# Kernel optimization log

Hardware: AMD Instinct MI355X
Metric: run time of the kernel (lower is better)

Reference implementation:

```python
import jax, jax.numpy as jnp
import numpy as np

D_MODEL, H, DK = 768, 12, 64
RQ, RK, RV = 6, 2, 2
B, S = 8, 4096


def setup_inputs() -> dict:
    key = jax.random.key(0)
    ks = jax.random.split(key, 16)
    def lin(k, din, dout):
        k1, k2 = jax.random.split(k)
        s = 1.0 / np.sqrt(din)
        W = jax.random.uniform(k1, (din, dout), jnp.float32, -s, s)
        b = jax.random.uniform(k2, (dout,), jnp.float32, -s, s)
        return W, b
    W_a_q, b_a_q = lin(ks[0], D_MODEL, H * RQ)
    W_b_q, b_b_q = lin(ks[1], D_MODEL, DK * RQ)
    W_a_k, b_a_k = lin(ks[2], D_MODEL, H * RK)
    W_b_k, b_b_k = lin(ks[3], D_MODEL, DK * RK)
    W_a_v, b_a_v = lin(ks[4], D_MODEL, H * RV)
    W_b_v, b_b_v = lin(ks[5], D_MODEL, DK * RV)
    W_out, b_out = lin(ks[6], H * DK, D_MODEL)
    x = jax.random.normal(ks[7], (B, S, D_MODEL), jnp.float32)
    rope_pos = jax.random.normal(ks[8], (S, DK), jnp.float32)
    return {
        "x": x, "rope_pos": rope_pos,
        "W_a_q": W_a_q, "b_a_q": b_a_q, "W_b_q": W_b_q, "b_b_q": b_b_q,
        "W_a_k": W_a_k, "b_a_k": b_a_k, "W_b_k": W_b_k, "b_b_k": b_b_k,
        "W_a_v": W_a_v, "b_a_v": b_a_v, "W_b_v": W_b_v, "b_b_v": b_b_v,
        "W_out": W_out, "b_out": b_out,
    }


def reference(x, rope_pos, W_a_q, b_a_q, W_b_q, b_b_q, W_a_k, b_a_k,
              W_b_k, b_b_k, W_a_v, b_a_v, W_b_v, b_b_v, W_out, b_out):
    b, s, _ = x.shape
    # factor projections; layout (B, S, rank, feature)
    A_Q = (x @ W_a_q + b_a_q).reshape(b, s, RQ, H)
    B_Q = (x @ W_b_q + b_b_q).reshape(b, s, RQ, DK)
    A_K = (x @ W_a_k + b_a_k).reshape(b, s, RK, H)
    B_K = (x @ W_b_k + b_b_k).reshape(b, s, RK, DK)
    A_V = (x @ W_a_v + b_a_v).reshape(b, s, RV, H)
    B_V = (x @ W_b_v + b_b_v).reshape(b, s, RV, DK)
    rope = rope_pos[None, :, None, :]  # (1,S,1,DK)
    B_Q = B_Q * rope
    B_K = B_K * rope
    # rank-sum outer products -> (B,S,H,DK)
    Q = jnp.einsum('bsrh,bsrd->bshd', A_Q, B_Q)
    K = jnp.einsum('bsrh,bsrd->bshd', A_K, B_K)
    V = jnp.einsum('bsrh,bsrd->bshd', A_V, B_V)
    # faithful to original: scores over head dim, shape (B,S,H,H)
    scores = jnp.einsum('bshd,bsgd->bshg', Q, K) / jnp.sqrt(jnp.float32(DK))
    attn = jax.nn.softmax(scores, axis=-1)
    out = jnp.einsum('bshg,bsgd->bshd', attn, V)  # (B,S,H,DK)
    # faithful reshape: (B,S,H,DK) -> transpose(1,2) -> (B,H,S,DK) -> view (B,S,H*DK)
    out = jnp.transpose(out, (0, 2, 1, 3)).reshape(b, s, H * DK)
    return out @ W_out + b_out
```

## Files before the change

### kernel.cpp

```cpp
#include <hip/hip_runtime.h>
#include <hip/hip_bf16.h>

#define D_MODEL 768
#define NH 12
#define DK 64
#define RQ 6
#define RK 2
#define RV 2
#define BATCH 8
#define SEQ 4096
#define NPOS (BATCH*SEQ)

typedef _Float16 v8h __attribute__((ext_vector_type(8)));
typedef float v4f __attribute__((ext_vector_type(4)));

#define GLDS16(ldst, gsrc)                                                     \
    __builtin_amdgcn_global_load_lds(                                          \
        (const __attribute__((address_space(1))) void*)(unsigned long long)    \
            (const void*)(gsrc),                                               \
        (__attribute__((address_space(3))) void*)(unsigned int)                \
            (unsigned long long)(void*)(ldst),                                 \
        16, 0, 0)

#define VMCNT(n) asm volatile("s_waitcnt vmcnt(" #n ")" ::: "memory")

__global__ __launch_bounds__(256) void repack(
    const float* __restrict__ Waq, const float* __restrict__ baq,
    const float* __restrict__ Wbq, const float* __restrict__ bbq,
    const float* __restrict__ Wak, const float* __restrict__ bak,
    const float* __restrict__ Wbk, const float* __restrict__ bbk,
    const float* __restrict__ Wav, const float* __restrict__ bav,
    const float* __restrict__ Wbv, const float* __restrict__ bbv,
    const float* __restrict__ Wo,
    _Float16* __restrict__ WcatT, _Float16* __restrict__ WoT,
    float* __restrict__ bcat)
{
    const int n = blockIdx.x;
    const int t = threadIdx.x;
    const float* W = nullptr; const float* bsrc = nullptr;
    int cols = 0, col = 0;
    if      (n <  72) { W=Waq; bsrc=baq; cols=72;  col=n;     }
    else if (n < 456) { W=Wbq; bsrc=bbq; cols=384; col=n-72;  }
    else if (n < 480) { W=Wak; bsrc=bak; cols=24;  col=n-456; }
    else if (n < 608) { W=Wbk; bsrc=bbk; cols=128; col=n-480; }
    else if (n < 632) { W=Wav; bsrc=bav; cols=24;  col=n-608; }
    else if (n < 760) { W=Wbv; bsrc=bbv; cols=128; col=n-632; }
    for (int k = t; k < 768; k += 256) {
        WcatT[(size_t)n*768 + k] = W ? (_Float16)W[(size_t)k*cols + col] : (_Float16)0.f;
        WoT[(size_t)n*768 + k]   = (_Float16)Wo[(size_t)k*768 + n];
    }
    if (t == 0) bcat[n] = W ? bsrc[col] : 0.f;
}

__global__ __launch_bounds__(256) void convert_x(
    const float4* __restrict__ x, v8h* __restrict__ xh)
{
    const int nth = gridDim.x * 256;
    for (int i = blockIdx.x*256 + threadIdx.x; i < NPOS*96; i += nth) {
        float4 a = x[2*(size_t)i];
        float4 b = x[2*(size_t)i + 1];
        v8h h;
        h[0]=(_Float16)a.x; h[1]=(_Float16)a.y; h[2]=(_Float16)a.z; h[3]=(_Float16)a.w;
        h[4]=(_Float16)b.x; h[5]=(_Float16)b.y; h[6]=(_Float16)b.z; h[7]=(_Float16)b.w;
        xh[i] = h;
    }
}

template<int MODE>
__global__ __launch_bounds__(256, 2) void mfma_gemm(
    const _Float16* __restrict__ A,
    const _Float16* __restrict__ BT,
    const float* __restrict__ bias,
    const float* __restrict__ rope,
    float* __restrict__ C)
{
    const int t = threadIdx.x;
    const int lane = t & 63;
    const int wave = t >> 6;

    const int flat = blockIdx.y * 6 + blockIdx.x;
    const int xcd = flat & 7;
    const int sub = flat >> 3;
    const int ct  = sub % 6;
    const int rt  = xcd * 32 + sub / 6;
    const int row0 = rt * 128;
    const int col0 = ct * 128;

    const int wrow = (wave >> 1) * 64;
    const int wcol = (wave & 1) * 64;

    __shared__ v8h SH[4][2][512];

    v4f acc[4][4];
    #pragma unroll
    for (int i = 0; i < 4; ++i)
        #pragma unroll
        for (int j = 0; j < 4; ++j)
            acc[i][j] = (v4f){0.f, 0.f, 0.f, 0.f};

    const v8h* gA = (const v8h*)A;
    const v8h* gB = (const v8h*)BT;

    const size_t gaW = (size_t)(row0 + wrow + (lane>>2))*96 + (lane&3);
    const size_t gbW = (size_t)(col0 + wcol + (lane>>2))*96 + (lane&3);
    char* ldsW = (char*)&SH[wave][0][0] + lane*16;

    const int q = lane >> 4;
    const int m = lane & 15;
    const int abase = m*4 + q;
    const int bbase = 256 + m*4 + q;

#define STAGE(b, ks) do {                                                      \
    _Pragma("unroll")                                                          \
    for (int j_ = 0; j_ < 4; ++j_)                                             \
        GLDS16(ldsW + (b)*8192 + j_*1024,        gA + gaW + (ks)*4 + j_*1536); \
    _Pragma("unroll")                                                          \
    for (int j_ = 0; j_ < 4; ++j_)                                             \
        GLDS16(ldsW + (b)*8192 + 4096 + j_*1024, gB + gbW + (ks)*4 + j_*1536); \
} while (0)

#define CMP(b) do {                                                            \
    v8h af[4], bf[4];                                                          \
    _Pragma("unroll")                                                          \
    for (int i_ = 0; i_ < 4; ++i_) af[i_] = SH[wave][b][abase + i_*64];        \
    _Pragma("unroll")                                                          \
    for (int i_ = 0; i_ < 4; ++i_) bf[i_] = SH[wave][b][bbase + i_*64];        \
    asm volatile("s_waitcnt lgkmcnt(0)" ::: "memory");                         \
    __builtin_amdgcn_sched_barrier(0);                                         \
    __builtin_amdgcn_s_setprio(1);                                             \
    _Pragma("unroll")                                                          \
    for (int mi_ = 0; mi_ < 4; ++mi_)                                          \
        _Pragma("unroll")                                                      \
        for (int ni_ = 0; ni_ < 4; ++ni_)                                      \
            acc[mi_][ni_] = __builtin_amdgcn_mfma_f32_16x16x32_f16(            \
                af[mi_], bf[ni_], acc[mi_][ni_], 0, 0, 0);                     \
    __builtin_amdgcn_s_setprio(0);                                             \
    asm volatile("" ::: "memory");                                             \
} while (0)

    STAGE(0, 0);
    for (int ks2 = 0; ks2 < 11; ++ks2) {
        STAGE(1, 2*ks2 + 1);
        VMCNT(8);
        CMP(0);
        STAGE(0, 2*ks2 + 2);
        VMCNT(8);
        CMP(1);
    }
    STAGE(1, 23);
    VMCNT(8);
    CMP(0);
    VMCNT(0);
    CMP(1);

#undef STAGE
#undef CMP

    #pragma unroll
    for (int mi = 0; mi < 4; ++mi) {
        #pragma unroll
        for (int i = 0; i < 4; ++i) {
            const int grow = row0 + wrow + mi*16 + q*4 + i;
            #pragma unroll
            for (int ni = 0; ni < 4; ++ni) {
                const int gcol = col0 + wcol + ni*16 + m;
                float v = acc[mi][ni][i] + bias[gcol];
                if (MODE == 0) {
                    const int s = grow & 4095;
                    if (gcol >= 72 && gcol < 456)
                        v *= rope[s*64 + ((gcol - 72) & 63)];
                    else if (gcol >= 480 && gcol < 608)
                        v *= rope[s*64 + ((gcol - 480) & 63)];
                }
                C[(size_t)grow*768 + gcol] = v;
            }
        }
    }
}

__global__ __launch_bounds__(256) void tpa_attn_f(
    const float* __restrict__ P,
    _Float16* __restrict__ O)
{
    const int t = threadIdx.x;
    const int pos0 = blockIdx.x * 8;

    __shared__ float proj[8][772];
    __shared__ float Gs[8][12];
    __shared__ float sc[8][160];
    __shared__ float cs[8][24];

    const float4* gp = (const float4*)P;
    for (int i = t; i < 8*192; i += 256) {
        int p = i / 192, c = i - p*192;
        float4 u = gp[(size_t)(pos0 + p)*192 + c];
        proj[p][c*4+0] = u.x; proj[p][c*4+1] = u.y;
        proj[p][c*4+2] = u.z; proj[p][c*4+3] = u.w;
    }
    __syncthreads();

    if (t < 96) {
        int p = t / 12, u = t - (t/12)*12, r = u >> 1, r2 = u & 1;
        const float* bq = &proj[p][72  + r*64];
        const float* bk = &proj[p][480 + r2*64];
        const int ph = (r*8 + r2*16) & 63;
        float acc = 0.f;
        for (int i = 0; i < 64; ++i) {
            int d = (i + ph) & 63;
            acc = fmaf(bq[d], bk[d], acc);
        }
        Gs[p][u] = acc * 0.125f;
    }
    __syncthreads();

    for (int i = t; i < 8*144; i += 256) {
        int p = i / 144, v = i - p*144, h = v / 12, g = v - (v/12)*12;
        float s = 0.f;
        #pragma unroll
        for (int r = 0; r < RQ; ++r) {
            float mg = fmaf(Gs[p][r*2+1], proj[p][468 + g],
                            Gs[p][r*2+0] * proj[p][456 + g]);
            s = fmaf(proj[p][r*12 + h], mg, s);
        }
        sc[p][h*13 + g] = s;
    }
    __syncthreads();

    if (t < 96) {
        int p = t / 12, h = t - (t/12)*12;
        float* row = &sc[p][h*13];
        float mx = -1e30f;
        #pragma unroll
        for (int g = 0; g < NH; ++g) mx = fmaxf(mx, row[g]);
        float sum = 0.f;
        #pragma unroll
        for (int g = 0; g < NH; ++g) { float e = __expf(row[g]-mx); row[g] = e; sum += e; }
        float inv = 1.0f / sum;
        #pragma unroll
        for (int g = 0; g < NH; ++g) row[g] *= inv;
    }
    __syncthreads();

    if (t < 192) {
        int p = t / 24, u = t - (t/24)*24, h = u >> 1, r2 = u & 1;
        float acc = 0.f;
        #pragma unroll
        for (int g = 0; g < NH; ++g)
            acc = fmaf(sc[p][h*13+g], proj[p][608 + r2*12 + g], acc);
        cs[p][h*2 + r2] = acc;
    }
    __syncthreads();

    for (int i = t; i < 8*768; i += 256) {
        int p = i / 768, j = i - p*768, h = j >> 6, d = j & 63;
        int pos = pos0 + p, b = pos >> 12, s = pos & 4095;
        float val = fmaf(cs[p][h*2+1], proj[p][632 + 64 + d],
                         cs[p][h*2+0] * proj[p][632 + d]);
        O[(((size_t)b*NH + h)*SEQ + s)*DK + d] = (_Float16)val;
    }
}

extern "C" void kernel_launch(void* const* d_in, const int* in_sizes, int n_in,
                              void* d_out, int out_size, void* d_ws, size_t ws_size,
                              hipStream_t stream) {
    const float* x    = (const float*)d_in[0];
    const float* rope = (const float*)d_in[1];
    const float* Waq  = (const float*)d_in[2];
    const float* baq  = (const float*)d_in[3];
    const float* Wbq  = (const float*)d_in[4];
    const float* bbq  = (const float*)d_in[5];
    const float* Wak  = (const float*)d_in[6];
    const float* bak  = (const float*)d_in[7];
    const float* Wbk  = (const float*)d_in[8];
    const float* bbk  = (const float*)d_in[9];
    const float* Wav  = (const float*)d_in[10];
    const float* bav  = (const float*)d_in[11];
    const float* Wbv  = (const float*)d_in[12];
    const float* bbv  = (const float*)d_in[13];
    const float* Wo   = (const float*)d_in[14];
    const float* bo   = (const float*)d_in[15];

    char* ws = (char*)d_ws;
    _Float16* WcatT = (_Float16*)(ws);
    _Float16* WoT   = (_Float16*)(ws + 1179648);
    float*    bcat  = (float*)(ws + 2359296);
    _Float16* O     = (_Float16*)(ws + 2363392);

    float* P = (float*)d_out;

    _Float16* Xh = O;

    repack<<<768, 256, 0, stream>>>(Waq, baq, Wbq, bbq, Wak, bak, Wbk, bbk,
                                    Wav, bav, Wbv, bbv, Wo, WcatT, WoT, bcat);

    convert_x<<<1024, 256, 0, stream>>>((const float4*)x, (v8h*)Xh);

    dim3 gg(6, 256);
    mfma_gemm<0><<<gg, 256, 0, stream>>>(Xh, WcatT, bcat, rope, P);

    tpa_attn_f<<<NPOS/8, 256, 0, stream>>>(P, O);

    mfma_gemm<1><<<gg, 256, 0, stream>>>(O, WoT, bo, nullptr, (float*)d_out);
}
```

Before: 411.7 us.

## Retile GEMM to 64-row blocks spanning all 768 columns with shared A tile

Restructures the MFMA GEMM so each 512-thread block computes a 64x768 output strip. Eight waves each own a 96-column panel and share one LDS-staged A tile, instead of six separate 128x128 tiles per row block. This is meant to cut repeated reads of the activation matrix and improve reuse, at the cost of block-wide barriers each k-step and lower occupancy (one block per CU, larger LDS).

```diff
diff --git a/kernel.cpp b/kernel.cpp
--- a/kernel.cpp
+++ b/kernel.cpp
@@ -23,6 +23,9 @@
         16, 0, 0)
 
 #define VMCNT(n) asm volatile("s_waitcnt vmcnt(" #n ")" ::: "memory")
+#define BAR() do { asm volatile("" ::: "memory");                              \
+                   __builtin_amdgcn_s_barrier();                               \
+                   asm volatile("" ::: "memory"); } while (0)
 
 __global__ __launch_bounds__(256) void repack(
     const float* __restrict__ Waq, const float* __restrict__ baq,
@@ -67,7 +70,7 @@
 }
 
 template<int MODE>
-__global__ __launch_bounds__(256, 2) void mfma_gemm(
+__global__ __launch_bounds__(512, 1) void mfma_gemm(
     const _Float16* __restrict__ A,
     const _Float16* __restrict__ BT,
     const float* __restrict__ bias,
@@ -78,92 +81,84 @@
     const int lane = t & 63;
     const int wave = t >> 6;
 
-    const int flat = blockIdx.y * 6 + blockIdx.x;
-    const int xcd = flat & 7;
-    const int sub = flat >> 3;
-    const int ct  = sub % 6;
-    const int rt  = xcd * 32 + sub / 6;
-    const int row0 = rt * 128;
-    const int col0 = ct * 128;
-
-    const int wrow = (wave >> 1) * 64;
-    const int wcol = (wave & 1) * 64;
-
-    __shared__ v8h SH[4][2][512];
-
-    v4f acc[4][4];
+    const int flat = blockIdx.x;
+    const int rt = (flat & 7) * 64 + (flat >> 3);
+    const int row0 = rt * 64;
+
+    __shared__ v8h Asl[2][256];
+    __shared__ v8h Bsl[2][8][384];
+
+    v4f acc[4][6];
     #pragma unroll
     for (int i = 0; i < 4; ++i)
         #pragma unroll
-        for (int j = 0; j < 4; ++j)
+        for (int j = 0; j < 6; ++j)
             acc[i][j] = (v4f){0.f, 0.f, 0.f, 0.f};
 
     const v8h* gA = (const v8h*)A;
     const v8h* gB = (const v8h*)BT;
 
-    const size_t gaW = (size_t)(row0 + wrow + (lane>>2))*96 + (lane&3);
-    const size_t gbW = (size_t)(col0 + wcol + (lane>>2))*96 + (lane&3);
-    char* ldsW = (char*)&SH[wave][0][0] + lane*16;
+    const size_t gaL = (size_t)(row0 + lane)*96 + wave;
+
+    const int colPan = wave * 96;
+    size_t gbL[6];
+    #pragma unroll
+    for (int j = 0; j < 6; ++j) {
+        int slot = j*64 + lane;
+        int kcB  = slot / 96;
+        int colB = slot - kcB*96;
+        gbL[j] = (size_t)(colPan + colB)*96 + kcB;
+    }
 
     const int q = lane >> 4;
     const int m = lane & 15;
-    const int abase = m*4 + q;
-    const int bbase = 256 + m*4 + q;
 
 #define STAGE(b, ks) do {                                                      \
     _Pragma("unroll")                                                          \
-    for (int j_ = 0; j_ < 4; ++j_)                                             \
-        GLDS16(ldsW + (b)*8192 + j_*1024,        gA + gaW + (ks)*4 + j_*1536); \
-    _Pragma("unroll")                                                          \
-    for (int j_ = 0; j_ < 4; ++j_)                                             \
-        GLDS16(ldsW + (b)*8192 + 4096 + j_*1024, gB + gbW + (ks)*4 + j_*1536); \
+    for (int j_ = 0; j_ < 6; ++j_)                                             \
+        GLDS16((char*)&Bsl[b][wave][j_*64] + lane*16, gB + gbL[j_] + (ks)*4);  \
+    if (wave < 4)                                                              \
+        GLDS16((char*)&Asl[b][wave*64] + lane*16, gA + gaL + (ks)*4);          \
 } while (0)
 
+#define WAITP() do { if (wave < 4) VMCNT(7); else VMCNT(6); } while (0)
+
 #define CMP(b) do {                                                            \
-    v8h af[4], bf[4];                                                          \
-    _Pragma("unroll")                                                          \
-    for (int i_ = 0; i_ < 4; ++i_) af[i_] = SH[wave][b][abase + i_*64];        \
-    _Pragma("unroll")                                                          \
-    for (int i_ = 0; i_ < 4; ++i_) bf[i_] = SH[wave][b][bbase + i_*64];        \
-    asm volatile("s_waitcnt lgkmcnt(0)" ::: "memory");                         \
-    __builtin_amdgcn_sched_barrier(0);                                         \
+    v8h af[4], bf[6];                                                          \
+    _Pragma("unroll")                                                          \
+    for (int i_ = 0; i_ < 4; ++i_) af[i_] = Asl[b][q*64 + i_*16 + m];          \
+    _Pragma("unroll")                                                          \
+    for (int i_ = 0; i_ < 6; ++i_) bf[i_] = Bsl[b][wave][q*96 + i_*16 + m];    \
     __builtin_amdgcn_s_setprio(1);                                             \
     _Pragma("unroll")                                                          \
     for (int mi_ = 0; mi_ < 4; ++mi_)                                          \
         _Pragma("unroll")                                                      \
-        for (int ni_ = 0; ni_ < 4; ++ni_)                                      \
+        for (int ni_ = 0; ni_ < 6; ++ni_)                                      \
             acc[mi_][ni_] = __builtin_amdgcn_mfma_f32_16x16x32_f16(            \
                 af[mi_], bf[ni_], acc[mi_][ni_], 0, 0, 0);                     \
     __builtin_amdgcn_s_setprio(0);                                             \
-    asm volatile("" ::: "memory");                                             \
 } while (0)
 
     STAGE(0, 0);
-    for (int ks2 = 0; ks2 < 11; ++ks2) {
-        STAGE(1, 2*ks2 + 1);
-        VMCNT(8);
-        CMP(0);
-        STAGE(0, 2*ks2 + 2);
-        VMCNT(8);
-        CMP(1);
-    }
-    STAGE(1, 23);
-    VMCNT(8);
-    CMP(0);
-    VMCNT(0);
-    CMP(1);
+    for (int u = 0; u < 11; ++u) {
+        STAGE(1, 2*u + 1); WAITP(); BAR(); CMP(0); BAR();
+        STAGE(0, 2*u + 2); WAITP(); BAR(); CMP(1); BAR();
+    }
+    STAGE(1, 23); WAITP(); BAR(); CMP(0); BAR();
+    VMCNT(0);            BAR(); CMP(1);
 
 #undef STAGE
+#undef WAITP
 #undef CMP
 
     #pragma unroll
     for (int mi = 0; mi < 4; ++mi) {
         #pragma unroll
         for (int i = 0; i < 4; ++i) {
-            const int grow = row0 + wrow + mi*16 + q*4 + i;
+            const int grow = row0 + mi*16 + q*4 + i;
             #pragma unroll
-            for (int ni = 0; ni < 4; ++ni) {
-                const int gcol = col0 + wcol + ni*16 + m;
+            for (int ni = 0; ni < 6; ++ni) {
+                const int gcol = colPan + ni*16 + m;
                 float v = acc[mi][ni][i] + bias[gcol];
                 if (MODE == 0) {
                     const int s = grow & 4095;
@@ -295,10 +290,9 @@
 
     convert_x<<<1024, 256, 0, stream>>>((const float4*)x, (v8h*)Xh);
 
-    dim3 gg(6, 256);
-    mfma_gemm<0><<<gg, 256, 0, stream>>>(Xh, WcatT, bcat, rope, P);
+    mfma_gemm<0><<<512, 512, 0, stream>>>(Xh, WcatT, bcat, rope, P);
 
     tpa_attn_f<<<NPOS/8, 256, 0, stream>>>(P, O);
 
-    mfma_gemm<1><<<gg, 256, 0, stream>>>(O, WoT, bo, nullptr, (float*)d_out);
-}
+    mfma_gemm<1><<<512, 512, 0, stream>>>(O, WoT, bo, nullptr, (float*)d_out);
+}
```

Measured after the change: 598.7 us. 45.4% more time.

## Share block-wide LDS tiles across waves with XOR swizzle and larger K-steps

Applied to the files above, without the earlier changes.

Previously each wave staged its own private 64x32 A and B slices, so each A row slice was loaded twice and each B slice twice per block. Now the whole block cooperatively stages 128x64 A and B tiles into shared LDS with an XOR swizzle, halving the number of K iterations and removing duplicate global traffic. The cost is block-wide barriers around each compute step, which serialise the waves, and a larger LDS footprint.

```diff
diff --git a/kernel.cpp b/kernel.cpp
--- a/kernel.cpp
+++ b/kernel.cpp
@@ -23,6 +23,9 @@
         16, 0, 0)
 
 #define VMCNT(n) asm volatile("s_waitcnt vmcnt(" #n ")" ::: "memory")
+#define BAR() do { asm volatile("" ::: "memory");                              \
+                   __builtin_amdgcn_s_barrier();                               \
+                   asm volatile("" ::: "memory"); } while (0)
 
 __global__ __launch_bounds__(256) void repack(
     const float* __restrict__ Waq, const float* __restrict__ baq,
@@ -89,7 +92,8 @@
     const int wrow = (wave >> 1) * 64;
     const int wcol = (wave & 1) * 64;
 
-    __shared__ v8h SH[4][2][512];
+    __shared__ v8h As[2][1024];
+    __shared__ v8h Bs[2][1024];
 
     v4f acc[4][4];
     #pragma unroll
@@ -101,57 +105,56 @@
     const v8h* gA = (const v8h*)A;
     const v8h* gB = (const v8h*)BT;
 
-    const size_t gaW = (size_t)(row0 + wrow + (lane>>2))*96 + (lane&3);
-    const size_t gbW = (size_t)(col0 + wcol + (lane>>2))*96 + (lane&3);
-    char* ldsW = (char*)&SH[wave][0][0] + lane*16;
+    const int srow = t >> 3;
+    const int skc  = (t & 7) ^ (srow & 7);
+    size_t gaJ[4], gbJ[4];
+    #pragma unroll
+    for (int j = 0; j < 4; ++j) {
+        gaJ[j] = (size_t)(row0 + j*32 + srow)*96 + skc;
+        gbJ[j] = (size_t)(col0 + j*32 + srow)*96 + skc;
+    }
 
     const int q = lane >> 4;
     const int m = lane & 15;
-    const int abase = m*4 + q;
-    const int bbase = 256 + m*4 + q;
+    const int mx = m & 7;
 
 #define STAGE(b, ks) do {                                                      \
     _Pragma("unroll")                                                          \
     for (int j_ = 0; j_ < 4; ++j_)                                             \
-        GLDS16(ldsW + (b)*8192 + j_*1024,        gA + gaW + (ks)*4 + j_*1536); \
+        GLDS16((char*)&As[b][0] + j_*4096 + t*16, gA + gaJ[j_] + (ks)*8);      \
     _Pragma("unroll")                                                          \
     for (int j_ = 0; j_ < 4; ++j_)                                             \
-        GLDS16(ldsW + (b)*8192 + 4096 + j_*1024, gB + gbW + (ks)*4 + j_*1536); \
+        GLDS16((char*)&Bs[b][0] + j_*4096 + t*16, gB + gbJ[j_] + (ks)*8);      \
 } while (0)
 
 #define CMP(b) do {                                                            \
-    v8h af[4], bf[4];                                                          \
     _Pragma("unroll")                                                          \
-    for (int i_ = 0; i_ < 4; ++i_) af[i_] = SH[wave][b][abase + i_*64];        \
-    _Pragma("unroll")                                                          \
-    for (int i_ = 0; i_ < 4; ++i_) bf[i_] = SH[wave][b][bbase + i_*64];        \
-    asm volatile("s_waitcnt lgkmcnt(0)" ::: "memory");                         \
-    __builtin_amdgcn_sched_barrier(0);                                         \
-    __builtin_amdgcn_s_setprio(1);                                             \
-    _Pragma("unroll")                                                          \
-    for (int mi_ = 0; mi_ < 4; ++mi_)                                          \
+    for (int ki_ = 0; ki_ < 2; ++ki_) {                                        \
+        v8h af[4], bf[4];                                                      \
         _Pragma("unroll")                                                      \
-        for (int ni_ = 0; ni_ < 4; ++ni_)                                      \
-            acc[mi_][ni_] = __builtin_amdgcn_mfma_f32_16x16x32_f16(            \
-                af[mi_], bf[ni_], acc[mi_][ni_], 0, 0, 0);                     \
-    __builtin_amdgcn_s_setprio(0);                                             \
-    asm volatile("" ::: "memory");                                             \
+        for (int i_ = 0; i_ < 4; ++i_)                                         \
+            af[i_] = As[b][(wrow + i_*16 + m)*8 + ((ki_*4 + q) ^ mx)];         \
+        _Pragma("unroll")                                                      \
+        for (int i_ = 0; i_ < 4; ++i_)                                         \
+            bf[i_] = Bs[b][(wcol + i_*16 + m)*8 + ((ki_*4 + q) ^ mx)];         \
+        __builtin_amdgcn_s_setprio(1);                                         \
+        _Pragma("unroll")                                                      \
+        for (int mi_ = 0; mi_ < 4; ++mi_)                                      \
+            _Pragma("unroll")                                                  \
+            for (int ni_ = 0; ni_ < 4; ++ni_)                                  \
+                acc[mi_][ni_] = __builtin_amdgcn_mfma_f32_16x16x32_f16(        \
+                    af[mi_], bf[ni_], acc[mi_][ni_], 0, 0, 0);                 \
+        __builtin_amdgcn_s_setprio(0);                                         \
+    }                                                                          \
 } while (0)
 
     STAGE(0, 0);
-    for (int ks2 = 0; ks2 < 11; ++ks2) {
-        STAGE(1, 2*ks2 + 1);
-        VMCNT(8);
-        CMP(0);
-        STAGE(0, 2*ks2 + 2);
-        VMCNT(8);
-        CMP(1);
-    }
-    STAGE(1, 23);
-    VMCNT(8);
-    CMP(0);
-    VMCNT(0);
-    CMP(1);
+    for (int u = 0; u < 5; ++u) {
+        STAGE(1, 2*u + 1); VMCNT(8); BAR(); CMP(0); BAR();
+        STAGE(0, 2*u + 2); VMCNT(8); BAR(); CMP(1); BAR();
+    }
+    STAGE(1, 11); VMCNT(8); BAR(); CMP(0); BAR();
+    VMCNT(0);               BAR(); CMP(1);
 
 #undef STAGE
 #undef CMP
```

Measured after the change: 374.4 us. 1.1x faster.
